# Performance work log

Hardware: AMD Instinct MI355X
Metric: run time of the kernel (lower is better)

The kernel has to match this reference:

```python
import jax, jax.numpy as jnp
import numpy as np

N, L, S, H, D = 2, 4096, 4096, 8, 64


def setup_inputs() -> dict:
    key = jax.random.key(0)
    kq, kk, kv = jax.random.split(key, 3)
    queries = jax.random.normal(kq, (N, L, H, D), dtype=jnp.float32)
    keys = jax.random.normal(kk, (N, S, H, D), dtype=jnp.float32)
    values = jax.random.normal(kv, (N, S, H, D), dtype=jnp.float32)
    return {"queries": queries, "keys": keys, "values": values}


def reference(queries, keys, values):
    # Full (non-fused) scaled dot-product attention, LoFTR FullAttention.
    # QK: [N, L, S, H]
    softmax_temp = 1.0 / jnp.sqrt(jnp.asarray(queries.shape[3], queries.dtype))
    QK = jnp.einsum('nlhd,nshd->nlsh', queries, keys)
    A = jax.nn.softmax(softmax_temp * QK, axis=2)  # softmax over S
    out = jnp.einsum('nlsh,nshd->nlhd', A, values)  # [N, L, H, D]
    return out
```

## Files before the change

### kernel.cpp

```cpp
#include <hip/hip_runtime.h>
#include <hip/hip_bf16.h>

typedef float  f32x4  __attribute__((ext_vector_type(4)));
typedef float  f32x16 __attribute__((ext_vector_type(16)));
typedef short  short8 __attribute__((ext_vector_type(8)));
typedef int    i32x2  __attribute__((ext_vector_type(2)));
typedef unsigned int uint4v __attribute__((ext_vector_type(4)));

#define N_  2
#define L_  4096
#define S_  4096
#define H_  8
#define D_  64
#define HD_ 512
#define KVB 64
#define QB  128
#define NT  (S_ / KVB)

__device__ __forceinline__ unsigned short f2bf(float f) {
  unsigned int u = __builtin_bit_cast(unsigned int, f);
  u += 0x7fffu + ((u >> 16) & 1u);
  return (unsigned short)(u >> 16);
}
__device__ __forceinline__ unsigned short bf16c(float f) {
  return __builtin_bit_cast(unsigned short, __float2bfloat16(f));
}
__device__ __forceinline__ unsigned int pk2(float lo, float hi) {
  unsigned int r;
  asm("v_cvt_pk_bf16_f32 %0, %1, %2" : "=v"(r) : "v"(lo), "v"(hi));
  return r;
}
__device__ __forceinline__ f32x16 zero16() {
  f32x16 v;
  #pragma unroll
  for (int i = 0; i < 16; ++i) v[i] = 0.f;
  return v;
}

#define GLD16(gp, lp)                                                          \
  __builtin_amdgcn_global_load_lds(                                            \
      (const __attribute__((address_space(1))) unsigned int*)(gp),             \
      (__attribute__((address_space(3))) unsigned int*)(lp), 16, 0, 0)

__global__ __launch_bounds__(256, 8)
void prepack(const float* __restrict__ Kg, const float* __restrict__ Vg,
             unsigned short* __restrict__ Kw, unsigned short* __restrict__ Vw) {
  const int b = blockIdx.x;
  const int tid = threadIdx.x;
  const int isV = (b >= 1024);
  const int tb = isV ? b - 1024 : b;
  const int nh = tb >> 6, t = tb & 63;
  const int n = nh >> 3, h = nh & 7;

  if (!isV) {
    const int sl = tid >> 2, d0 = (tid & 3) << 4;
    const float* src = Kg + ((size_t)(n * S_ + t * 64 + sl) * H_ + h) * D_ + d0;
    f32x4 x0 = *(const f32x4*)(src);
    f32x4 x1 = *(const f32x4*)(src + 4);
    f32x4 x2 = *(const f32x4*)(src + 8);
    f32x4 x3 = *(const f32x4*)(src + 12);
    short8 t0, t1;
    t0[0] = (short)f2bf(x0[0]); t0[1] = (short)f2bf(x0[1]);
    t0[2] = (short)f2bf(x0[2]); t0[3] = (short)f2bf(x0[3]);
    t0[4] = (short)f2bf(x1[0]); t0[5] = (short)f2bf(x1[1]);
    t0[6] = (short)f2bf(x1[2]); t0[7] = (short)f2bf(x1[3]);
    t1[0] = (short)f2bf(x2[0]); t1[1] = (short)f2bf(x2[1]);
    t1[2] = (short)f2bf(x2[2]); t1[3] = (short)f2bf(x2[3]);
    t1[4] = (short)f2bf(x3[0]); t1[5] = (short)f2bf(x3[1]);
    t1[6] = (short)f2bf(x3[2]); t1[7] = (short)f2bf(x3[3]);
    unsigned short* dst = Kw + (size_t)tb * 4096 + sl * 64;
    const int b0 = d0 >> 3;
    *(short8*)&dst[((b0)     ^ (sl & 7)) * 8] = t0;
    *(short8*)&dst[((b0 + 1) ^ (sl & 7)) * 8] = t1;
  } else {
    const int d = tid & 63, sb2 = tid >> 6;
    const int fd = d & 7;
    #pragma unroll
    for (int c = 0; c < 2; ++c) {
      const int sblk = sb2 * 2 + c;
      const float* src = Vg + ((size_t)(n * S_ + t * 64 + sblk * 8) * H_ + h) * D_ + d;
      short8 o;
      #pragma unroll
      for (int j = 0; j < 8; ++j) o[j] = (short)f2bf(src[(size_t)j * HD_]);
      *(short8*)&Vw[(size_t)tb * 4096 + d * 64 + (sblk ^ fd) * 8] = o;
    }
  }
}

__global__ __launch_bounds__(256, 2)
void attn_fa3(const float* __restrict__ Qg,
              const unsigned short* __restrict__ Kw,
              const unsigned short* __restrict__ Vw,
              float* __restrict__ Og) {
  __shared__ __align__(16) unsigned short Kl[2][KVB * D_];
  __shared__ __align__(16) unsigned short Vl[2][D_ * KVB];

  const int tid = threadIdx.x;
  const int wv  = tid >> 6;
  const int ln  = tid & 63;
  const int hi  = ln >> 5;
  const int c32 = ln & 31;

  const int bid = blockIdx.x;
  const int swz = (bid & 7) * 64 + (bid >> 3);
  const int qt  = swz & 31;
  const int nh  = swz >> 5;
  const int h = nh & 7, n = nh >> 3;
  const int qbase = qt * QB;

  const float qs = 0.125f * 1.44269504088896340736f;
  const int qrow = qbase + (wv << 5) + c32;
  const float* qp = Qg + (size_t)(n * L_ + qrow) * HD_ + h * D_ + (hi << 3);
  short8 qf[4];
  #pragma unroll
  for (int kc = 0; kc < 4; ++kc) {
    const float* p = qp + (kc << 4);
    f32x4 a = *(const f32x4*)(p);
    f32x4 b = *(const f32x4*)(p + 4);
    short8 f;
    f[0] = (short)bf16c(a[0] * qs); f[1] = (short)bf16c(a[1] * qs);
    f[2] = (short)bf16c(a[2] * qs); f[3] = (short)bf16c(a[3] * qs);
    f[4] = (short)bf16c(b[0] * qs); f[5] = (short)bf16c(b[1] * qs);
    f[6] = (short)bf16c(b[2] * qs); f[7] = (short)bf16c(b[3] * qs);
    qf[kc] = f;
  }
  asm volatile("s_waitcnt vmcnt(0)" ::: "memory");

  f32x16 acc0 = zero16(), acc1 = zero16();
  float lsum = 0.f;

  const char* Kt = (const char*)(Kw + (size_t)nh * 64 * 4096);
  const char* Vt = (const char*)(Vw + (size_t)nh * 64 * 4096);
  const size_t lo = (size_t)(wv << 10) + (ln << 4);

  GLD16(Kt + lo,        &Kl[0][wv << 9]);
  GLD16(Kt + lo + 4096, &Kl[0][2048 + (wv << 9)]);
  GLD16(Vt + lo,        &Vl[0][wv << 9]);
  GLD16(Vt + lo + 4096, &Vl[0][2048 + (wv << 9)]);

  for (int t = 0; t < NT; ++t) {
    const int cur = t & 1;
    if (t + 1 < NT) {
      const size_t off = (size_t)(t + 1) * 8192 + lo;
      GLD16(Kt + off,        &Kl[cur ^ 1][wv << 9]);
      GLD16(Kt + off + 4096, &Kl[cur ^ 1][2048 + (wv << 9)]);
      GLD16(Vt + off,        &Vl[cur ^ 1][wv << 9]);
      GLD16(Vt + off + 4096, &Vl[cur ^ 1][2048 + (wv << 9)]);
      asm volatile("s_waitcnt vmcnt(4)" ::: "memory");
    } else {
      asm volatile("s_waitcnt vmcnt(0)" ::: "memory");
    }
    __builtin_amdgcn_s_barrier();

    const unsigned short* Kb = Kl[cur];
    const unsigned short* Vb = Vl[cur];

    short8 kf0[4], kf1[4];
    #pragma unroll
    for (int kc = 0; kc < 4; ++kc) {
      const int ph = (((kc << 1) | hi) ^ (c32 & 7)) * 8;
      kf0[kc] = *(const short8*)&Kb[c32 * 64 + ph];
      kf1[kc] = *(const short8*)&Kb[(32 + c32) * 64 + ph];
    }

    f32x16 s0a = zero16(), s1a = zero16();
    __builtin_amdgcn_s_setprio(1);
    #pragma unroll
    for (int kc = 0; kc < 4; ++kc) {
      s0a = __builtin_amdgcn_mfma_f32_32x32x16_bf16(kf0[kc], qf[kc], s0a, 0, 0, 0);
      s1a = __builtin_amdgcn_mfma_f32_32x32x16_bf16(kf1[kc], qf[kc], s1a, 0, 0, 0);
    }
    __builtin_amdgcn_s_setprio(0);

    short8 vf[4][2];
    #pragma unroll
    for (int sc = 0; sc < 4; ++sc) {
      const int ph = (((sc << 1) | hi) ^ (c32 & 7)) * 8;
      vf[sc][0] = *(const short8*)&Vb[c32 * 64 + ph];
      vf[sc][1] = *(const short8*)&Vb[(32 + c32) * 64 + ph];
    }

    #pragma unroll
    for (int r = 0; r < 16; ++r) {
      s0a[r] = __builtin_amdgcn_exp2f(s0a[r]); lsum += s0a[r];
    }
    #pragma unroll
    for (int r = 0; r < 16; ++r) {
      s1a[r] = __builtin_amdgcn_exp2f(s1a[r]); lsum += s1a[r];
    }

    #pragma unroll
    for (int sc = 0; sc < 4; ++sc) {
      const int c = sc & 1;
      unsigned int c0, c1, c2, c3;
      if (sc < 2) {
        c0 = pk2(s0a[8 * c + 0], s0a[8 * c + 1]);
        c1 = pk2(s0a[8 * c + 2], s0a[8 * c + 3]);
        c2 = pk2(s0a[8 * c + 4], s0a[8 * c + 5]);
        c3 = pk2(s0a[8 * c + 6], s0a[8 * c + 7]);
      } else {
        c0 = pk2(s1a[8 * c + 0], s1a[8 * c + 1]);
        c1 = pk2(s1a[8 * c + 2], s1a[8 * c + 3]);
        c2 = pk2(s1a[8 * c + 4], s1a[8 * c + 5]);
        c3 = pk2(s1a[8 * c + 6], s1a[8 * c + 7]);
      }
      i32x2 r0 = __builtin_amdgcn_permlane32_swap((int)c0, (int)c2, false, false);
      i32x2 r1 = __builtin_amdgcn_permlane32_swap((int)c1, (int)c3, false, false);
      uint4v w = { (unsigned)r0[0], (unsigned)r1[0], (unsigned)r0[1], (unsigned)r1[1] };
      const short8 pa = __builtin_bit_cast(short8, w);
      __builtin_amdgcn_s_setprio(1);
      acc0 = __builtin_amdgcn_mfma_f32_32x32x16_bf16(pa, vf[sc][0], acc0, 0, 0, 0);
      acc1 = __builtin_amdgcn_mfma_f32_32x32x16_bf16(pa, vf[sc][1], acc1, 0, 0, 0);
      __builtin_amdgcn_s_setprio(0);
    }

    asm volatile("s_waitcnt lgkmcnt(0)" ::: "memory");
    __builtin_amdgcn_s_barrier();
  }

  const float full = lsum + __shfl_xor(lsum, 32);
  #pragma unroll
  for (int r = 0; r < 16; ++r) {
    const int qsrc = (r & 3) + 8 * (r >> 2) + 4 * hi;
    const float l = __shfl(full, qsrc);
    const float inv = 1.f / l;
    const int row = qbase + (wv << 5) + qsrc;
    float* op = Og + (size_t)(n * L_ + row) * HD_ + h * D_ + c32;
    op[0]  = acc0[r] * inv;
    op[32] = acc1[r] * inv;
  }
}

extern "C" void kernel_launch(void* const* d_in, const int* in_sizes, int n_in,
                              void* d_out, int out_size, void* d_ws, size_t ws_size,
                              hipStream_t stream) {
  (void)in_sizes; (void)n_in; (void)out_size; (void)ws_size;
  const float* Q = (const float*)d_in[0];
  const float* K = (const float*)d_in[1];
  const float* V = (const float*)d_in[2];
  float* O = (float*)d_out;

  unsigned short* Kw = (unsigned short*)d_ws;
  unsigned short* Vw = Kw + 4194304;
  hipLaunchKernelGGL(prepack, dim3(2048), dim3(256), 0, stream, K, V, Kw, Vw);
  hipLaunchKernelGGL(attn_fa3, dim3(512), dim3(256), 0, stream, Q, Kw, Vw, O);
}
```

Before: 95.82 us.

## Load V fragments directly from global into registers and restructure K pipeline

```diff
diff --git a/kernel.cpp b/kernel.cpp
--- a/kernel.cpp
+++ b/kernel.cpp
@@ -74,7 +74,6 @@
     *(short8*)&dst[((b0 + 1) ^ (sl & 7)) * 8] = t1;
   } else {
     const int d = tid & 63, sb2 = tid >> 6;
-    const int fd = d & 7;
     #pragma unroll
     for (int c = 0; c < 2; ++c) {
       const int sblk = sb2 * 2 + c;
@@ -82,18 +81,96 @@
       short8 o;
       #pragma unroll
       for (int j = 0; j < 8; ++j) o[j] = (short)f2bf(src[(size_t)j * HD_]);
-      *(short8*)&Vw[(size_t)tb * 4096 + d * 64 + (sblk ^ fd) * 8] = o;
+      *(short8*)&Vw[(size_t)tb * 4096 + sblk * 512 + d * 8] = o;
     }
   }
 }
 
+template<int W1, int W2, int DOK, int DOV>
+__device__ __forceinline__ void tile_body(
+    int t, const int hi, const int c32, const int wv,
+    const char* Kt, const char* Vt, const size_t klane, const size_t vlane,
+    unsigned short (*Kl)[KVB * D_],
+    const short8 qf[4], const short8* vc, short8* vn,
+    f32x16& acc0, f32x16& acc1, float& lsum)
+{
+  const int cur = t & 1;
+  asm volatile("s_waitcnt vmcnt(%0)" :: "n"(W1) : "memory");
+  __builtin_amdgcn_s_barrier();
+  const unsigned short* Kb = Kl[cur];
+
+  short8 kf0[4], kf1[4];
+  #pragma unroll
+  for (int kc = 0; kc < 4; ++kc) {
+    const int ph = (((kc << 1) | hi) ^ (c32 & 7)) * 8;
+    kf0[kc] = *(const short8*)&Kb[c32 * 64 + ph];
+    kf1[kc] = *(const short8*)&Kb[(32 + c32) * 64 + ph];
+  }
+
+  f32x16 s0a = zero16(), s1a = zero16();
+  __builtin_amdgcn_s_setprio(1);
+  #pragma unroll
+  for (int kc = 0; kc < 4; ++kc) {
+    s0a = __builtin_amdgcn_mfma_f32_32x32x16_bf16(kf0[kc], qf[kc], s0a, 0, 0, 0);
+    s1a = __builtin_amdgcn_mfma_f32_32x32x16_bf16(kf1[kc], qf[kc], s1a, 0, 0, 0);
+  }
+  __builtin_amdgcn_s_setprio(0);
+
+  asm volatile("s_waitcnt lgkmcnt(0)" ::: "memory");
+  __builtin_amdgcn_s_barrier();
+
+  if (DOK) {
+    const char* kp = Kt + (size_t)(t + 2) * 8192 + klane;
+    GLD16(kp,        &Kl[cur][wv << 9]);
+    GLD16(kp + 4096, &Kl[cur][2048 + (wv << 9)]);
+  }
+  if (DOV) {
+    const char* vp = Vt + (size_t)(t + 1) * 8192 + vlane;
+    #pragma unroll
+    for (int q8 = 0; q8 < 8; ++q8)
+      vn[q8] = *(const short8*)(vp + (q8 >> 1) * 2048 + (q8 & 1) * 512);
+  }
+
+  #pragma unroll
+  for (int r = 0; r < 16; ++r) { s0a[r] = __builtin_amdgcn_exp2f(s0a[r]); lsum += s0a[r]; }
+  #pragma unroll
+  for (int r = 0; r < 16; ++r) { s1a[r] = __builtin_amdgcn_exp2f(s1a[r]); lsum += s1a[r]; }
+
+  asm volatile("s_waitcnt vmcnt(%0)" :: "n"(W2) : "memory");
+  __builtin_amdgcn_sched_barrier(0);
+
+  #pragma unroll
+  for (int sc = 0; sc < 4; ++sc) {
+    const int c = sc & 1;
+    unsigned int c0, c1, c2, c3;
+    if (sc < 2) {
+      c0 = pk2(s0a[8 * c + 0], s0a[8 * c + 1]);
+      c1 = pk2(s0a[8 * c + 2], s0a[8 * c + 3]);
+      c2 = pk2(s0a[8 * c + 4], s0a[8 * c + 5]);
+      c3 = pk2(s0a[8 * c + 6], s0a[8 * c + 7]);
+    } else {
+      c0 = pk2(s1a[8 * c + 0], s1a[8 * c + 1]);
+      c1 = pk2(s1a[8 * c + 2], s1a[8 * c + 3]);
+      c2 = pk2(s1a[8 * c + 4], s1a[8 * c + 5]);
+      c3 = pk2(s1a[8 * c + 6], s1a[8 * c + 7]);
+    }
+    i32x2 r0 = __builtin_amdgcn_permlane32_swap((int)c0, (int)c2, false, false);
+    i32x2 r1 = __builtin_amdgcn_permlane32_swap((int)c1, (int)c3, false, false);
+    uint4v w = { (unsigned)r0[0], (unsigned)r1[0], (unsigned)r0[1], (unsigned)r1[1] };
+    const short8 pa = __builtin_bit_cast(short8, w);
+    __builtin_amdgcn_s_setprio(1);
+    acc0 = __builtin_amdgcn_mfma_f32_32x32x16_bf16(pa, vc[sc * 2 + 0], acc0, 0, 0, 0);
+    acc1 = __builtin_amdgcn_mfma_f32_32x32x16_bf16(pa, vc[sc * 2 + 1], acc1, 0, 0, 0);
+    __builtin_amdgcn_s_setprio(0);
+  }
+}
+
 __global__ __launch_bounds__(256, 2)
-void attn_fa3(const float* __restrict__ Qg,
+void attn_fa4(const float* __restrict__ Qg,
               const unsigned short* __restrict__ Kw,
               const unsigned short* __restrict__ Vw,
               float* __restrict__ Og) {
   __shared__ __align__(16) unsigned short Kl[2][KVB * D_];
-  __shared__ __align__(16) unsigned short Vl[2][D_ * KVB];
 
   const int tid = threadIdx.x;
   const int wv  = tid >> 6;
@@ -131,92 +208,28 @@
 
   const char* Kt = (const char*)(Kw + (size_t)nh * 64 * 4096);
   const char* Vt = (const char*)(Vw + (size_t)nh * 64 * 4096);
-  const size_t lo = (size_t)(wv << 10) + (ln << 4);
-
-  GLD16(Kt + lo,        &Kl[0][wv << 9]);
-  GLD16(Kt + lo + 4096, &Kl[0][2048 + (wv << 9)]);
-  GLD16(Vt + lo,        &Vl[0][wv << 9]);
-  GLD16(Vt + lo + 4096, &Vl[0][2048 + (wv << 9)]);
-
-  for (int t = 0; t < NT; ++t) {
-    const int cur = t & 1;
-    if (t + 1 < NT) {
-      const size_t off = (size_t)(t + 1) * 8192 + lo;
-      GLD16(Kt + off,        &Kl[cur ^ 1][wv << 9]);
-      GLD16(Kt + off + 4096, &Kl[cur ^ 1][2048 + (wv << 9)]);
-      GLD16(Vt + off,        &Vl[cur ^ 1][wv << 9]);
-      GLD16(Vt + off + 4096, &Vl[cur ^ 1][2048 + (wv << 9)]);
-      asm volatile("s_waitcnt vmcnt(4)" ::: "memory");
-    } else {
-      asm volatile("s_waitcnt vmcnt(0)" ::: "memory");
-    }
-    __builtin_amdgcn_s_barrier();
-
-    const unsigned short* Kb = Kl[cur];
-    const unsigned short* Vb = Vl[cur];
-
-    short8 kf0[4], kf1[4];
+  const size_t klane = (size_t)((wv << 10) + (ln << 4));
+  const size_t vlane = (size_t)((hi << 10) + (c32 << 4));
+
+  short8 vA[8], vB[8];
+
+  GLD16(Kt + klane,               &Kl[0][wv << 9]);
+  GLD16(Kt + klane + 4096,        &Kl[0][2048 + (wv << 9)]);
+  GLD16(Kt + 8192 + klane,        &Kl[1][wv << 9]);
+  GLD16(Kt + 8192 + klane + 4096, &Kl[1][2048 + (wv << 9)]);
+  {
+    const char* vp = Vt + vlane;
     #pragma unroll
-    for (int kc = 0; kc < 4; ++kc) {
-      const int ph = (((kc << 1) | hi) ^ (c32 & 7)) * 8;
-      kf0[kc] = *(const short8*)&Kb[c32 * 64 + ph];
-      kf1[kc] = *(const short8*)&Kb[(32 + c32) * 64 + ph];
-    }
-
-    f32x16 s0a = zero16(), s1a = zero16();
-    __builtin_amdgcn_s_setprio(1);
-    #pragma unroll
-    for (int kc = 0; kc < 4; ++kc) {
-      s0a = __builtin_amdgcn_mfma_f32_32x32x16_bf16(kf0[kc], qf[kc], s0a, 0, 0, 0);
-      s1a = __builtin_amdgcn_mfma_f32_32x32x16_bf16(kf1[kc], qf[kc], s1a, 0, 0, 0);
-    }
-    __builtin_amdgcn_s_setprio(0);
-
-    short8 vf[4][2];
-    #pragma unroll
-    for (int sc = 0; sc < 4; ++sc) {
-      const int ph = (((sc << 1) | hi) ^ (c32 & 7)) * 8;
-      vf[sc][0] = *(const short8*)&Vb[c32 * 64 + ph];
-      vf[sc][1] = *(const short8*)&Vb[(32 + c32) * 64 + ph];
-    }
-
-    #pragma unroll
-    for (int r = 0; r < 16; ++r) {
-      s0a[r] = __builtin_amdgcn_exp2f(s0a[r]); lsum += s0a[r];
-    }
-    #pragma unroll
-    for (int r = 0; r < 16; ++r) {
-      s1a[r] = __builtin_amdgcn_exp2f(s1a[r]); lsum += s1a[r];
-    }
-
-    #pragma unroll
-    for (int sc = 0; sc < 4; ++sc) {
-      const int c = sc & 1;
-      unsigned int c0, c1, c2, c3;
-      if (sc < 2) {
-        c0 = pk2(s0a[8 * c + 0], s0a[8 * c + 1]);
-        c1 = pk2(s0a[8 * c + 2], s0a[8 * c + 3]);
-        c2 = pk2(s0a[8 * c + 4], s0a[8 * c + 5]);
-        c3 = pk2(s0a[8 * c + 6], s0a[8 * c + 7]);
-      } else {
-        c0 = pk2(s1a[8 * c + 0], s1a[8 * c + 1]);
-        c1 = pk2(s1a[8 * c + 2], s1a[8 * c + 3]);
-        c2 = pk2(s1a[8 * c + 4], s1a[8 * c + 5]);
-        c3 = pk2(s1a[8 * c + 6], s1a[8 * c + 7]);
-      }
-      i32x2 r0 = __builtin_amdgcn_permlane32_swap((int)c0, (int)c2, false, false);
-      i32x2 r1 = __builtin_amdgcn_permlane32_swap((int)c1, (int)c3, false, false);
-      uint4v w = { (unsigned)r0[0], (unsigned)r1[0], (unsigned)r0[1], (unsigned)r1[1] };
-      const short8 pa = __builtin_bit_cast(short8, w);
-      __builtin_amdgcn_s_setprio(1);
-      acc0 = __builtin_amdgcn_mfma_f32_32x32x16_bf16(pa, vf[sc][0], acc0, 0, 0, 0);
-      acc1 = __builtin_amdgcn_mfma_f32_32x32x16_bf16(pa, vf[sc][1], acc1, 0, 0, 0);
-      __builtin_amdgcn_s_setprio(0);
-    }
-
-    asm volatile("s_waitcnt lgkmcnt(0)" ::: "memory");
-    __builtin_amdgcn_s_barrier();
-  }
+    for (int q8 = 0; q8 < 8; ++q8)
+      vA[q8] = *(const short8*)(vp + (q8 >> 1) * 2048 + (q8 & 1) * 512);
+  }
+
+  for (int t = 0; t < NT - 2; t += 2) {
+    tile_body<10, 10, 1, 1>(t,     hi, c32, wv, Kt, Vt, klane, vlane, Kl, qf, vA, vB, acc0, acc1, lsum);
+    tile_body<10, 10, 1, 1>(t + 1, hi, c32, wv, Kt, Vt, klane, vlane, Kl, qf, vB, vA, acc0, acc1, lsum);
+  }
+  tile_body<10, 8, 0, 1>(NT - 2, hi, c32, wv, Kt, Vt, klane, vlane, Kl, qf, vA, vB, acc0, acc1, lsum);
+  tile_body< 8, 0, 0, 0>(NT - 1, hi, c32, wv, Kt, Vt, klane, vlane, Kl, qf, vB, vA, acc0, acc1, lsum);
 
   const float full = lsum + __shfl_xor(lsum, 32);
   #pragma unroll
@@ -243,5 +256,5 @@
   unsigned short* Kw = (unsigned short*)d_ws;
   unsigned short* Vw = Kw + 4194304;
   hipLaunchKernelGGL(prepack, dim3(2048), dim3(256), 0, stream, K, V, Kw, Vw);
-  hipLaunchKernelGGL(attn_fa3, dim3(512), dim3(256), 0, stream, Q, Kw, Vw, O);
-}
+  hipLaunchKernelGGL(attn_fa4, dim3(512), dim3(256), 0, stream, Q, Kw, Vw, O);
+}
```

New measurement: 95.30 us. About the same (-0.5%).
